# Performance work log

Measured on AMD Instinct MI355X. Metric: run time of the kernel, lower is better.

Reference implementation:

```python
import jax, jax.numpy as jnp
import numpy as np

# ---- static config (mirrors init_kwargs) ----
WIN_X, WIN_Y = 12, 12
GRID_X, GRID_Y = 468, 468
BATCH = 4
SHIFTS = ((0, 0), (6, 6))
MAX_WIN_X = GRID_X // WIN_X + 1            # 40
MAX_WIN_Y = GRID_Y // WIN_Y + 1            # 40
MAX_WIN_PER_SAMPLE = MAX_WIN_X * MAX_WIN_Y # 1600
# (level, max_tokens, drop_range_lo, drop_range_hi)
DROP_INFO = ((0, 30, 0, 30), (1, 60, 30, 60), (2, 100, 60, 100000))
SENTINEL = 2_000_000_000  # window id for masked-out voxels (sorts to the end)


def _window_partition(coors):
    # coors: [N,4] = [b, z, y, x] int32 -> batch-unique window index per shift
    out = []
    for sx, sy in SHIFTS:
        x = coors[:, 3] + sx
        y = coors[:, 2] + sy
        wx = x // WIN_X
        wy = y // WIN_Y
        out.append((coors[:, 0] * MAX_WIN_PER_SAMPLE + wx * MAX_WIN_Y + wy).astype(jnp.int32))
    return out


def _sort_group_stats(win):
    # inner index within each equal-value group (counting-sort style) and group size per element
    order = jnp.argsort(win)                      # stable
    s = win[order]
    n = win.shape[0]
    left_s = jnp.searchsorted(s, s, side='left')
    inner_sorted = jnp.arange(n, dtype=win.dtype) - left_s.astype(win.dtype)
    inner = jnp.zeros_like(win).at[order].set(inner_sorted)
    counts = (jnp.searchsorted(s, win, side='right') - jnp.searchsorted(s, win, side='left')).astype(win.dtype)
    return inner, counts


def _drop_single_shift(win, valid):
    # equivalent of SSTInputLayer.drop_single_shift restricted to `valid` voxels
    w = jnp.where(valid, win, SENTINEL)
    inner, counts = _sort_group_stats(w)
    target = jnp.zeros_like(w)
    lvl = -jnp.ones_like(w)
    for dl, max_tok, lo, hi in DROP_INFO:
        m = (counts >= lo) & (counts < hi)
        target = jnp.where(m, max_tok, target)
        lvl = jnp.where(m, dl, lvl)
    keep = valid & (inner < target)
    return keep, jnp.where(valid, lvl, -1)


def _make_continuous(w):
    # dense-rank of window ids (make_continuous_inds) over a sentinel-masked array
    order = jnp.argsort(w)
    s = w[order]
    new_grp = jnp.concatenate([jnp.zeros((1,), w.dtype), (s[1:] != s[:-1]).astype(w.dtype)])
    rank = jnp.cumsum(new_grp)
    return jnp.zeros_like(w).at[order].set(rank)


def _flat2win(win, keep, lvl):
    # per-voxel position in the [num_windows, max_tokens] buffer of its drop level; -1 if dropped
    out = -jnp.ones_like(win)
    for dl, max_tok, _, _ in DROP_INFO:
        valid = keep & (lvl == dl)
        w = jnp.where(valid, win, SENTINEL)
        conti = _make_continuous(w)
        inner, _ = _sort_group_stats(w)
        out = jnp.where(valid, conti * max_tok + inner, out)
    return out


def reference(voxel_feat, coors):
    coors = coors.astype(jnp.int32)
    bwi0, bwi1 = _window_partition(coors)
    n = voxel_feat.shape[0]
    all_valid = jnp.ones((n,), bool)
    keep0, lvl0 = _drop_single_shift(bwi0, all_valid)
    keep1, lvl1 = _drop_single_shift(bwi1, keep0)   # shift-1 drop computed among shift-0 survivors
    keep = keep0 & keep1
    feat = jnp.where(keep[:, None], voxel_feat, 0.0)  # fixed-shape analogue of voxel_feat[voxel_keep_inds]
    f2w0 = _flat2win(bwi0, keep, lvl0)
    f2w1 = _flat2win(bwi1, keep, lvl1)
    return feat, keep, lvl0, lvl1, bwi0, bwi1, f2w0, f2w1


def setup_inputs() -> dict:
    key = jax.random.key(0)
    k1, k2, k3, k4 = jax.random.split(key, 4)
    n, c = 300000, 128
    voxel_feat = jax.random.normal(k1, (n, c), dtype=jnp.float32)
    b = jax.random.randint(k2, (n,), 0, BATCH)
    y = jax.random.randint(k3, (n,), 0, GRID_Y)
    x = jax.random.randint(k4, (n,), 0, GRID_X)
    z = jnp.zeros((n,), jnp.int32)
    coors = jnp.stack([b, z, y, x], axis=1).astype(jnp.int32)
    return {"voxel_feat": voxel_feat, "coors": coors}
```

## Files before the change

### kernel.cpp

```cpp
#include <hip/hip_runtime.h>


#define NWIN 6400
#define SEG_CAP 3072

__global__ void k_zero(int* __restrict__ hdr, int* __restrict__ keepF, int n) {
    int i = blockIdx.x * blockDim.x + threadIdx.x;
    if (i < 4 * NWIN) hdr[i] = 0;
    if (i < n) keepF[i] = 0;
}

__global__ void k_windows(const int* __restrict__ coors, int n,
                          int* __restrict__ w0a, int* __restrict__ w1a,
                          int* __restrict__ cnt0) {
    int i = blockIdx.x * blockDim.x + threadIdx.x;
    if (i >= n) return;
    int b = coors[4 * i];
    int y = coors[4 * i + 2];
    int x = coors[4 * i + 3];
    int w0 = b * 1600 + (x / 12) * 40 + (y / 12);
    int w1 = b * 1600 + ((x + 6) / 12) * 40 + ((y + 6) / 12);
    w0a[i] = w0;
    w1a[i] = w1;
    atomicAdd(&cnt0[w0], 1);
}

__global__ void k_scan(const int* __restrict__ cnt, int* __restrict__ base,
                       int* __restrict__ lvlW) {
    __shared__ int psum[256];
    int t = threadIdx.x;
    int st = t * 25;
    int s = 0;
    for (int j = 0; j < 25; j++) s += cnt[st + j];
    psum[t] = s;
    __syncthreads();
    if (t == 0) {
        int acc = 0;
        for (int j = 0; j < 256; j++) { int v = psum[j]; psum[j] = acc; acc += v; }
    }
    __syncthreads();
    int acc = psum[t];
    for (int j = 0; j < 25; j++) {
        int w = st + j;
        int c = cnt[w];
        base[w] = acc;
        acc += c;
        int lvl;
        if (c < 30) lvl = 0;
        else if (c < 60) lvl = 1;
        else if (c < 100000) lvl = 2;
        else lvl = -1;
        lvlW[w] = lvl;
    }
}

__global__ void k_count_masked(const int* __restrict__ wa, const int* __restrict__ mask,
                               int n, int* __restrict__ cnt) {
    int i = blockIdx.x * blockDim.x + threadIdx.x;
    if (i >= n) return;
    if (!mask[i]) return;
    atomicAdd(&cnt[wa[i]], 1);
}

__global__ void k_scatter(const int* __restrict__ wa, const int* __restrict__ mask, int n,
                          const int* __restrict__ base, int* __restrict__ cur,
                          int* __restrict__ seg) {
    int i = blockIdx.x * blockDim.x + threadIdx.x;
    if (i >= n) return;
    if (mask && !mask[i]) return;
    int w = wa[i];
    int p = atomicAdd(&cur[w], 1);
    seg[base[w] + p] = i;
}

__global__ void k_rankkeep(const int* __restrict__ cnt, const int* __restrict__ base,
                           const int* __restrict__ seg, int* __restrict__ keepOut) {
    int w = blockIdx.x;
    int k = cnt[w];
    if (k == 0) return;
    int bs = base[w];
    int target;
    if (k < 30) target = 30;
    else if (k < 60) target = 60;
    else if (k < 100000) target = 100;
    else target = 0;
    __shared__ int lds[SEG_CAP];
    if (k <= SEG_CAP) {
        for (int j = threadIdx.x; j < k; j += blockDim.x) lds[j] = seg[bs + j];
        __syncthreads();
        for (int e = threadIdx.x; e < k; e += blockDim.x) {
            int v = lds[e];
            int r = 0;
            for (int j = 0; j < k; j++) r += (lds[j] < v) ? 1 : 0;
            keepOut[v] = (r < target) ? 1 : 0;
        }
    } else {
        for (int e = threadIdx.x; e < k; e += blockDim.x) {
            int v = seg[bs + e];
            int r = 0;
            for (int j = 0; j < k; j++) r += (seg[bs + j] < v) ? 1 : 0;
            keepOut[v] = (r < target) ? 1 : 0;
        }
    }
}

__global__ void k_rankkept(const int* __restrict__ cnt, const int* __restrict__ base,
                           const int* __restrict__ seg, const int* __restrict__ keepF,
                           int* __restrict__ rk, int* __restrict__ keptC) {
    int w = blockIdx.x;
    int k = cnt[w];
    __shared__ int lds[SEG_CAP];
    __shared__ int red[64];
    int local = 0;
    if (k > 0) {
        int bs = base[w];
        if (k <= SEG_CAP) {
            for (int j = threadIdx.x; j < k; j += blockDim.x) {
                int v = seg[bs + j];
                lds[j] = v | (keepF[v] << 30);
            }
            __syncthreads();
            for (int e = threadIdx.x; e < k; e += blockDim.x) {
                int enc = lds[e];
                int kept = enc >> 30;
                local += kept;
                if (!kept) continue;
                int v = enc & 0x3FFFFFFF;
                int r = 0;
                for (int j = 0; j < k; j++) {
                    int ej = lds[j];
                    r += (ej >> 30) & (int)((ej & 0x3FFFFFFF) < v);
                }
                rk[v] = r;
            }
        } else {
            for (int e = threadIdx.x; e < k; e += blockDim.x) {
                int v = seg[bs + e];
                int f = keepF[v];
                local += f;
                if (!f) continue;
                int r = 0;
                for (int j = 0; j < k; j++) {
                    int u = seg[bs + j];
                    r += (keepF[u] && (u < v)) ? 1 : 0;
                }
                rk[v] = r;
            }
        }
    }
    red[threadIdx.x] = local;
    __syncthreads();
    if (threadIdx.x == 0) {
        int s = 0;
        for (int j = 0; j < 64; j++) s += red[j];
        keptC[w] = s;
    }
}

__global__ void k_conti(const int* __restrict__ lvlW, const int* __restrict__ keptC,
                        int* __restrict__ conti) {
    __shared__ int pc0[256], pc1[256], pc2[256];
    int t = threadIdx.x;
    int st = t * 25;
    int c0 = 0, c1 = 0, c2 = 0;
    for (int j = 0; j < 25; j++) {
        int w = st + j;
        if (keptC[w] > 0) {
            int l = lvlW[w];
            c0 += (l == 0); c1 += (l == 1); c2 += (l == 2);
        }
    }
    pc0[t] = c0; pc1[t] = c1; pc2[t] = c2;
    __syncthreads();
    if (t == 0) {
        int a = 0, b = 0, c = 0;
        for (int j = 0; j < 256; j++) {
            int v0 = pc0[j], v1 = pc1[j], v2 = pc2[j];
            pc0[j] = a; pc1[j] = b; pc2[j] = c;
            a += v0; b += v1; c += v2;
        }
    }
    __syncthreads();
    int a0 = pc0[t], a1 = pc1[t], a2 = pc2[t];
    for (int j = 0; j < 25; j++) {
        int w = st + j;
        int l = lvlW[w];
        int cc = (l == 0) ? a0 : (l == 1) ? a1 : (l == 2) ? a2 : 0;
        conti[w] = cc;
        if (keptC[w] > 0) {
            if (l == 0) a0++; else if (l == 1) a1++; else if (l == 2) a2++;
        }
    }
}

__global__ void k_final(int n, const int* __restrict__ w0a, const int* __restrict__ w1a,
                        const int* __restrict__ keep0, const int* __restrict__ keepF,
                        const int* __restrict__ lvlW0, const int* __restrict__ lvlW1,
                        const int* __restrict__ conti0, const int* __restrict__ conti1,
                        const int* __restrict__ rk0, const int* __restrict__ rk1,
                        float* __restrict__ out) {
    int i = blockIdx.x * blockDim.x + threadIdx.x;
    if (i >= n) return;
    size_t N = (size_t)n;
    float* o = out + N * 128;
    int w0 = w0a[i], w1 = w1a[i];
    int k0 = keep0[i];
    int kf = keepF[i];
    int l0 = lvlW0[w0];
    int l1 = k0 ? lvlW1[w1] : -1;
    int f0 = -1, f1 = -1;
    if (kf) {
        int mt0 = (l0 == 0) ? 30 : (l0 == 1) ? 60 : 100;
        int mt1 = (l1 == 0) ? 30 : (l1 == 1) ? 60 : 100;
        f0 = conti0[w0] * mt0 + rk0[i];
        f1 = conti1[w1] * mt1 + rk1[i];
    }
    o[i]         = (float)kf;
    o[N + i]     = (float)l0;
    o[2 * N + i] = (float)l1;
    o[3 * N + i] = (float)w0;
    o[4 * N + i] = (float)w1;
    o[5 * N + i] = (float)f0;
    o[6 * N + i] = (float)f1;
}

__global__ void k_feat(const float4* __restrict__ in, const int* __restrict__ keepF,
                       float4* __restrict__ out, int n) {
    int gid = blockIdx.x * blockDim.x + threadIdx.x;
    int total = n * 32;
    if (gid >= total) return;
    int row = gid >> 5;
    float4 v = in[gid];
    if (!keepF[row]) { v.x = 0.f; v.y = 0.f; v.z = 0.f; v.w = 0.f; }
    out[gid] = v;
}

extern "C" void kernel_launch(void* const* d_in, const int* in_sizes, int n_in,
                              void* d_out, int out_size, void* d_ws, size_t ws_size,
                              hipStream_t stream) {
    (void)n_in; (void)out_size; (void)ws_size;
    const float* feat = (const float*)d_in[0];
    const int* coors  = (const int*)d_in[1];
    int n = in_sizes[1] / 4;
    float* out = (float*)d_out;
    int* ws = (int*)d_ws;

    int* cnt0   = ws;
    int* cur0   = ws + 6400;
    int* cnt1   = ws + 12800;
    int* cur1   = ws + 19200;
    int* base0  = ws + 25600;
    int* base1  = ws + 32000;
    int* lvlW0  = ws + 38400;
    int* lvlW1  = ws + 44800;
    int* keptC0 = ws + 51200;
    int* keptC1 = ws + 57600;
    int* conti0 = ws + 64000;
    int* conti1 = ws + 70400;
    int* w0a    = ws + 76800;
    int* w1a    = w0a + n;
    int* seg0   = w1a + n;
    int* seg1   = seg0 + n;
    int* keep0  = seg1 + n;
    int* keepF  = keep0 + n;
    int* rk0    = keepF + n;
    int* rk1    = rk0 + n;

    int nb = (n + 255) / 256;
    int zmax = (n > 4 * NWIN) ? n : 4 * NWIN;
    int zb = (zmax + 255) / 256;

    k_zero<<<zb, 256, 0, stream>>>(cnt0, keepF, n);
    k_windows<<<nb, 256, 0, stream>>>(coors, n, w0a, w1a, cnt0);
    k_scan<<<1, 256, 0, stream>>>(cnt0, base0, lvlW0);
    k_scatter<<<nb, 256, 0, stream>>>(w0a, (const int*)nullptr, n, base0, cur0, seg0);
    k_rankkeep<<<NWIN, 64, 0, stream>>>(cnt0, base0, seg0, keep0);
    k_count_masked<<<nb, 256, 0, stream>>>(w1a, keep0, n, cnt1);
    k_scan<<<1, 256, 0, stream>>>(cnt1, base1, lvlW1);
    k_scatter<<<nb, 256, 0, stream>>>(w1a, keep0, n, base1, cur1, seg1);
    k_rankkeep<<<NWIN, 64, 0, stream>>>(cnt1, base1, seg1, keepF);
    k_rankkept<<<NWIN, 64, 0, stream>>>(cnt0, base0, seg0, keepF, rk0, keptC0);
    k_rankkept<<<NWIN, 64, 0, stream>>>(cnt1, base1, seg1, keepF, rk1, keptC1);
    k_conti<<<1, 256, 0, stream>>>(lvlW0, keptC0, conti0);
    k_conti<<<1, 256, 0, stream>>>(lvlW1, keptC1, conti1);
    k_final<<<nb, 256, 0, stream>>>(n, w0a, w1a, keep0, keepF, lvlW0, lvlW1,
                                    conti0, conti1, rk0, rk1, out);
    int fb = (n * 32 + 255) / 256;
    k_feat<<<fb, 256, 0, stream>>>((const float4*)feat, keepF, (float4*)out, n);
}
```

Before: 438.9 us.

## Fuse all index-computation stages into one cooperative kernel with grid syncs

Replaces the fourteen small launches for window counting, scanning, scattering, ranking and the final index write with a single cooperative kernel of 512 blocks that separates stages with grid.sync(). It also folds the shift-1 count into the shift-0 rank pass and computes keptC1 inline, which removes one pass and one launch. The aim is to cut launch overhead and the idle tails of single-block scan kernels. In exchange, the ranking passes now run on fewer, larger blocks than the one-block-per-window layout, and each grid barrier has its own cost. The old multi-kernel path stays as a fallback if the cooperative launch fails.

```diff
diff --git a/kernel.cpp b/kernel.cpp
--- a/kernel.cpp
+++ b/kernel.cpp
@@ -1,8 +1,292 @@
 #include <hip/hip_runtime.h>
+#include <hip/hip_cooperative_groups.h>
+
+namespace cg = cooperative_groups;
 
 
 #define NWIN 6400
 #define SEG_CAP 3072
+#define CBLK 512
+#define CTHR 256
+
+
+__device__ __forceinline__ void scan6400(const int* __restrict__ cnt,
+                                         int* __restrict__ base,
+                                         int* __restrict__ lvlW,
+                                         int* psum) {
+    int t = threadIdx.x;
+    int st = t * 25;
+    int s = 0;
+    for (int j = 0; j < 25; j++) s += cnt[st + j];
+    psum[t] = s;
+    __syncthreads();
+    if (t == 0) {
+        int acc = 0;
+        for (int j = 0; j < 256; j++) { int v = psum[j]; psum[j] = acc; acc += v; }
+    }
+    __syncthreads();
+    int acc = psum[t];
+    for (int j = 0; j < 25; j++) {
+        int w = st + j;
+        int c = cnt[w];
+        base[w] = acc;
+        acc += c;
+        lvlW[w] = (c < 30) ? 0 : (c < 60) ? 1 : (c < 100000) ? 2 : -1;
+    }
+}
+
+__device__ __forceinline__ void conti6400(const int* __restrict__ lvlW,
+                                          const int* __restrict__ keptC,
+                                          int* __restrict__ conti,
+                                          int* pc0, int* pc1, int* pc2) {
+    int t = threadIdx.x;
+    int st = t * 25;
+    int c0 = 0, c1 = 0, c2 = 0;
+    for (int j = 0; j < 25; j++) {
+        int w = st + j;
+        if (keptC[w] > 0) {
+            int l = lvlW[w];
+            c0 += (l == 0); c1 += (l == 1); c2 += (l == 2);
+        }
+    }
+    pc0[t] = c0; pc1[t] = c1; pc2[t] = c2;
+    __syncthreads();
+    if (t == 0) {
+        int a = 0, b = 0, c = 0;
+        for (int j = 0; j < 256; j++) {
+            int v0 = pc0[j], v1 = pc1[j], v2 = pc2[j];
+            pc0[j] = a; pc1[j] = b; pc2[j] = c;
+            a += v0; b += v1; c += v2;
+        }
+    }
+    __syncthreads();
+    int a0 = pc0[t], a1 = pc1[t], a2 = pc2[t];
+    for (int j = 0; j < 25; j++) {
+        int w = st + j;
+        int l = lvlW[w];
+        conti[w] = (l == 0) ? a0 : (l == 1) ? a1 : (l == 2) ? a2 : 0;
+        if (keptC[w] > 0) {
+            if (l == 0) a0++; else if (l == 1) a1++; else if (l == 2) a2++;
+        }
+    }
+}
+
+__global__ void __launch_bounds__(CTHR, 2)
+k_coop(const int* __restrict__ coors, int n, int* __restrict__ ws,
+       float* __restrict__ out) {
+    cg::grid_group grid = cg::this_grid();
+
+    int* cnt0   = ws;
+    int* cur0   = ws + 6400;
+    int* cnt1   = ws + 12800;
+    int* cur1   = ws + 19200;
+    int* base0  = ws + 25600;
+    int* base1  = ws + 32000;
+    int* lvlW0  = ws + 38400;
+    int* lvlW1  = ws + 44800;
+    int* keptC0 = ws + 51200;
+    int* keptC1 = ws + 57600;
+    int* conti0 = ws + 64000;
+    int* conti1 = ws + 70400;
+    int* w0a    = ws + 76800;
+    int* w1a    = w0a + n;
+    int* seg0   = w1a + n;
+    int* seg1   = seg0 + n;
+    int* keep0  = seg1 + n;
+    int* keepF  = keep0 + n;
+    int* rk0    = keepF + n;
+    int* rk1    = rk0 + n;
+
+    __shared__ int lds[SEG_CAP];
+    __shared__ int red[256];
+    __shared__ int pcA[256], pcB[256], pcC[256];
+
+    const int tid  = threadIdx.x;
+    const int gid0 = blockIdx.x * CTHR + tid;
+    const int gs   = gridDim.x * CTHR;
+
+    for (int i = gid0; i < 4 * NWIN; i += gs) ws[i] = 0;
+    for (int i = gid0; i < n; i += gs) keepF[i] = 0;
+    grid.sync();
+
+    const int4* c4 = (const int4*)coors;
+    for (int i = gid0; i < n; i += gs) {
+        int4 c = c4[i];
+        int w0 = c.x * 1600 + (c.w / 12) * 40 + (c.z / 12);
+        int w1 = c.x * 1600 + ((c.w + 6) / 12) * 40 + ((c.z + 6) / 12);
+        w0a[i] = w0; w1a[i] = w1;
+        atomicAdd(&cnt0[w0], 1);
+    }
+    grid.sync();
+
+    if (blockIdx.x == 0) scan6400(cnt0, base0, lvlW0, red);
+    grid.sync();
+
+    for (int i = gid0; i < n; i += gs) {
+        int w = w0a[i];
+        int p = atomicAdd(&cur0[w], 1);
+        seg0[base0[w] + p] = i;
+    }
+    grid.sync();
+
+    for (int w = blockIdx.x; w < NWIN; w += gridDim.x) {
+        int k = cnt0[w];
+        if (k == 0) continue;
+        int bs = base0[w];
+        int target = (k < 30) ? 30 : (k < 60) ? 60 : (k < 100000) ? 100 : 0;
+        if (k <= SEG_CAP) {
+            for (int j = tid; j < k; j += CTHR) lds[j] = seg0[bs + j];
+            __syncthreads();
+            for (int e = tid; e < k; e += CTHR) {
+                int v = lds[e];
+                int r = 0;
+                for (int j = 0; j < k; j++) r += (lds[j] < v) ? 1 : 0;
+                int kp = (r < target) ? 1 : 0;
+                keep0[v] = kp;
+                if (kp) atomicAdd(&cnt1[w1a[v]], 1);
+            }
+            __syncthreads();
+        } else {
+            for (int e = tid; e < k; e += CTHR) {
+                int v = seg0[bs + e];
+                int r = 0;
+                for (int j = 0; j < k; j++) r += (seg0[bs + j] < v) ? 1 : 0;
+                int kp = (r < target) ? 1 : 0;
+                keep0[v] = kp;
+                if (kp) atomicAdd(&cnt1[w1a[v]], 1);
+            }
+        }
+    }
+    grid.sync();
+
+    if (blockIdx.x == 0) scan6400(cnt1, base1, lvlW1, red);
+    grid.sync();
+
+    for (int i = gid0; i < n; i += gs) {
+        if (!keep0[i]) continue;
+        int w = w1a[i];
+        int p = atomicAdd(&cur1[w], 1);
+        seg1[base1[w] + p] = i;
+    }
+    grid.sync();
+
+    for (int w = blockIdx.x; w < NWIN; w += gridDim.x) {
+        int k = cnt1[w];
+        int target = (k < 30) ? 30 : (k < 60) ? 60 : (k < 100000) ? 100 : 0;
+        if (tid == 0) keptC1[w] = (k < target) ? k : target;
+        if (k == 0) continue;
+        int bs = base1[w];
+        if (k <= SEG_CAP) {
+            for (int j = tid; j < k; j += CTHR) lds[j] = seg1[bs + j];
+            __syncthreads();
+            for (int e = tid; e < k; e += CTHR) {
+                int v = lds[e];
+                int r = 0;
+                for (int j = 0; j < k; j++) r += (lds[j] < v) ? 1 : 0;
+                if (r < target) { keepF[v] = 1; rk1[v] = r; }
+            }
+            __syncthreads();
+        } else {
+            for (int e = tid; e < k; e += CTHR) {
+                int v = seg1[bs + e];
+                int r = 0;
+                for (int j = 0; j < k; j++) r += (seg1[bs + j] < v) ? 1 : 0;
+                if (r < target) { keepF[v] = 1; rk1[v] = r; }
+            }
+        }
+    }
+    grid.sync();
+
+    for (int w = blockIdx.x; w < NWIN; w += gridDim.x) {
+        int k = cnt0[w];
+        int bs = base0[w];
+        int local = 0;
+        if (k > 0 && k <= SEG_CAP) {
+            for (int j = tid; j < k; j += CTHR) {
+                int v = seg0[bs + j];
+                lds[j] = v | (keepF[v] << 30);
+            }
+            __syncthreads();
+            for (int e = tid; e < k; e += CTHR) {
+                int enc = lds[e];
+                int kept = enc >> 30;
+                local += kept;
+                if (kept) {
+                    int v = enc & 0x3FFFFFFF;
+                    int r = 0;
+                    for (int j = 0; j < k; j++) {
+                        int ej = lds[j];
+                        r += (ej >> 30) & (int)((ej & 0x3FFFFFFF) < v);
+                    }
+                    rk0[v] = r;
+                }
+            }
+        } else if (k > 0) {
+            for (int e = tid; e < k; e += CTHR) {
+                int v = seg0[bs + e];
+                int f = keepF[v];
+                local += f;
+                if (f) {
+                    int r = 0;
+                    for (int j = 0; j < k; j++) {
+                        int u = seg0[bs + j];
+                        r += (keepF[u] && (u < v)) ? 1 : 0;
+                    }
+                    rk0[v] = r;
+                }
+            }
+        }
+        red[tid] = local;
+        __syncthreads();
+        if (tid == 0) {
+            int s = 0;
+            for (int j = 0; j < 256; j++) s += red[j];
+            keptC0[w] = s;
+        }
+        __syncthreads();
+    }
+    grid.sync();
+
+    if (blockIdx.x == 0)      conti6400(lvlW0, keptC0, conti0, pcA, pcB, pcC);
+    else if (blockIdx.x == 1) conti6400(lvlW1, keptC1, conti1, pcA, pcB, pcC);
+    grid.sync();
+
+    size_t N = (size_t)n;
+    float* o = out + N * 128;
+    for (int i = gid0; i < n; i += gs) {
+        int w0 = w0a[i], w1 = w1a[i];
+        int k0 = keep0[i];
+        int kf = keepF[i];
+        int l0 = lvlW0[w0];
+        int l1 = k0 ? lvlW1[w1] : -1;
+        int f0 = -1, f1 = -1;
+        if (kf) {
+            int mt0 = (l0 == 0) ? 30 : (l0 == 1) ? 60 : 100;
+            int mt1 = (l1 == 0) ? 30 : (l1 == 1) ? 60 : 100;
+            f0 = conti0[w0] * mt0 + rk0[i];
+            f1 = conti1[w1] * mt1 + rk1[i];
+        }
+        o[i]         = (float)kf;
+        o[N + i]     = (float)l0;
+        o[2 * N + i] = (float)l1;
+        o[3 * N + i] = (float)w0;
+        o[4 * N + i] = (float)w1;
+        o[5 * N + i] = (float)f0;
+        o[6 * N + i] = (float)f1;
+    }
+}
+
+__global__ void k_feat(const float4* __restrict__ in, const int* __restrict__ keepF,
+                       float4* __restrict__ out, int n) {
+    int gid = blockIdx.x * blockDim.x + threadIdx.x;
+    int total = n * 32;
+    if (gid >= total) return;
+    int row = gid >> 5;
+    float4 v = in[gid];
+    if (!keepF[row]) { v.x = 0.f; v.y = 0.f; v.z = 0.f; v.w = 0.f; }
+    out[gid] = v;
+}
+
 
 __global__ void k_zero(int* __restrict__ hdr, int* __restrict__ keepF, int n) {
     int i = blockIdx.x * blockDim.x + threadIdx.x;
@@ -28,30 +312,7 @@
 __global__ void k_scan(const int* __restrict__ cnt, int* __restrict__ base,
                        int* __restrict__ lvlW) {
     __shared__ int psum[256];
-    int t = threadIdx.x;
-    int st = t * 25;
-    int s = 0;
-    for (int j = 0; j < 25; j++) s += cnt[st + j];
-    psum[t] = s;
-    __syncthreads();
-    if (t == 0) {
-        int acc = 0;
-        for (int j = 0; j < 256; j++) { int v = psum[j]; psum[j] = acc; acc += v; }
-    }
-    __syncthreads();
-    int acc = psum[t];
-    for (int j = 0; j < 25; j++) {
-        int w = st + j;
-        int c = cnt[w];
-        base[w] = acc;
-        acc += c;
-        int lvl;
-        if (c < 30) lvl = 0;
-        else if (c < 60) lvl = 1;
-        else if (c < 100000) lvl = 2;
-        else lvl = -1;
-        lvlW[w] = lvl;
-    }
+    scan6400(cnt, base, lvlW, psum);
 }
 
 __global__ void k_count_masked(const int* __restrict__ wa, const int* __restrict__ mask,
@@ -160,37 +421,7 @@
 __global__ void k_conti(const int* __restrict__ lvlW, const int* __restrict__ keptC,
                         int* __restrict__ conti) {
     __shared__ int pc0[256], pc1[256], pc2[256];
-    int t = threadIdx.x;
-    int st = t * 25;
-    int c0 = 0, c1 = 0, c2 = 0;
-    for (int j = 0; j < 25; j++) {
-        int w = st + j;
-        if (keptC[w] > 0) {
-            int l = lvlW[w];
-            c0 += (l == 0); c1 += (l == 1); c2 += (l == 2);
-        }
-    }
-    pc0[t] = c0; pc1[t] = c1; pc2[t] = c2;
-    __syncthreads();
-    if (t == 0) {
-        int a = 0, b = 0, c = 0;
-        for (int j = 0; j < 256; j++) {
-            int v0 = pc0[j], v1 = pc1[j], v2 = pc2[j];
-            pc0[j] = a; pc1[j] = b; pc2[j] = c;
-            a += v0; b += v1; c += v2;
-        }
-    }
-    __syncthreads();
-    int a0 = pc0[t], a1 = pc1[t], a2 = pc2[t];
-    for (int j = 0; j < 25; j++) {
-        int w = st + j;
-        int l = lvlW[w];
-        int cc = (l == 0) ? a0 : (l == 1) ? a1 : (l == 2) ? a2 : 0;
-        conti[w] = cc;
-        if (keptC[w] > 0) {
-            if (l == 0) a0++; else if (l == 1) a1++; else if (l == 2) a2++;
-        }
-    }
+    conti6400(lvlW, keptC, conti, pc0, pc1, pc2);
 }
 
 __global__ void k_final(int n, const int* __restrict__ w0a, const int* __restrict__ w1a,
@@ -224,17 +455,6 @@
     o[6 * N + i] = (float)f1;
 }
 
-__global__ void k_feat(const float4* __restrict__ in, const int* __restrict__ keepF,
-                       float4* __restrict__ out, int n) {
-    int gid = blockIdx.x * blockDim.x + threadIdx.x;
-    int total = n * 32;
-    if (gid >= total) return;
-    int row = gid >> 5;
-    float4 v = in[gid];
-    if (!keepF[row]) { v.x = 0.f; v.y = 0.f; v.z = 0.f; v.w = 0.f; }
-    out[gid] = v;
-}
-
 extern "C" void kernel_launch(void* const* d_in, const int* in_sizes, int n_in,
                               void* d_out, int out_size, void* d_ws, size_t ws_size,
                               hipStream_t stream) {
@@ -266,25 +486,30 @@
     int* rk0    = keepF + n;
     int* rk1    = rk0 + n;
 
-    int nb = (n + 255) / 256;
-    int zmax = (n > 4 * NWIN) ? n : 4 * NWIN;
-    int zb = (zmax + 255) / 256;
-
-    k_zero<<<zb, 256, 0, stream>>>(cnt0, keepF, n);
-    k_windows<<<nb, 256, 0, stream>>>(coors, n, w0a, w1a, cnt0);
-    k_scan<<<1, 256, 0, stream>>>(cnt0, base0, lvlW0);
-    k_scatter<<<nb, 256, 0, stream>>>(w0a, (const int*)nullptr, n, base0, cur0, seg0);
-    k_rankkeep<<<NWIN, 64, 0, stream>>>(cnt0, base0, seg0, keep0);
-    k_count_masked<<<nb, 256, 0, stream>>>(w1a, keep0, n, cnt1);
-    k_scan<<<1, 256, 0, stream>>>(cnt1, base1, lvlW1);
-    k_scatter<<<nb, 256, 0, stream>>>(w1a, keep0, n, base1, cur1, seg1);
-    k_rankkeep<<<NWIN, 64, 0, stream>>>(cnt1, base1, seg1, keepF);
-    k_rankkept<<<NWIN, 64, 0, stream>>>(cnt0, base0, seg0, keepF, rk0, keptC0);
-    k_rankkept<<<NWIN, 64, 0, stream>>>(cnt1, base1, seg1, keepF, rk1, keptC1);
-    k_conti<<<1, 256, 0, stream>>>(lvlW0, keptC0, conti0);
-    k_conti<<<1, 256, 0, stream>>>(lvlW1, keptC1, conti1);
-    k_final<<<nb, 256, 0, stream>>>(n, w0a, w1a, keep0, keepF, lvlW0, lvlW1,
-                                    conti0, conti1, rk0, rk1, out);
+    void* kargs[4] = { (void*)&coors, (void*)&n, (void*)&ws, (void*)&out };
+    hipError_t err = hipLaunchCooperativeKernel((const void*)k_coop,
+                                                dim3(CBLK), dim3(CTHR),
+                                                kargs, 0, stream);
+    if (err != hipSuccess) {
+        int nb = (n + 255) / 256;
+        int zmax = (n > 4 * NWIN) ? n : 4 * NWIN;
+        int zb = (zmax + 255) / 256;
+        k_zero<<<zb, 256, 0, stream>>>(cnt0, keepF, n);
+        k_windows<<<nb, 256, 0, stream>>>(coors, n, w0a, w1a, cnt0);
+        k_scan<<<1, 256, 0, stream>>>(cnt0, base0, lvlW0);
+        k_scatter<<<nb, 256, 0, stream>>>(w0a, (const int*)nullptr, n, base0, cur0, seg0);
+        k_rankkeep<<<NWIN, 64, 0, stream>>>(cnt0, base0, seg0, keep0);
+        k_count_masked<<<nb, 256, 0, stream>>>(w1a, keep0, n, cnt1);
+        k_scan<<<1, 256, 0, stream>>>(cnt1, base1, lvlW1);
+        k_scatter<<<nb, 256, 0, stream>>>(w1a, keep0, n, base1, cur1, seg1);
+        k_rankkeep<<<NWIN, 64, 0, stream>>>(cnt1, base1, seg1, keepF);
+        k_rankkept<<<NWIN, 64, 0, stream>>>(cnt0, base0, seg0, keepF, rk0, keptC0);
+        k_rankkept<<<NWIN, 64, 0, stream>>>(cnt1, base1, seg1, keepF, rk1, keptC1);
+        k_conti<<<1, 256, 0, stream>>>(lvlW0, keptC0, conti0);
+        k_conti<<<1, 256, 0, stream>>>(lvlW1, keptC1, conti1);
+        k_final<<<nb, 256, 0, stream>>>(n, w0a, w1a, keep0, keepF, lvlW0, lvlW1,
+                                        conti0, conti1, rk0, rk1, out);
+    }
     int fb = (n * 32 + 255) / 256;
     k_feat<<<fb, 256, 0, stream>>>((const float4*)feat, keepF, (float4*)out, n);
 }
```

New measurement: 1.035 ms. 2.36x slower.
